# Kernel tuning notes

Hardware: AMD Instinct MI355X
Metric: run time of the kernel (lower is better)

The kernel has to match this reference:

```python
import jax, jax.numpy as jnp
import numpy as np

SCALE = 0.08838834764831845  # 1/sqrt(head_dim=128)


def setup_inputs() -> dict:
    key = jax.random.key(0)
    ks = jax.random.split(key, 5)
    B, H, D = 16, 8, 128          # batch (decode seqs), kv heads, head_dim
    BS, BPS = 16, 128             # block_size, blocks per sequence
    NBLK = B * BPS                # total cache blocks (2048)
    CTX = 2048                    # context length per sequence
    q = jax.random.normal(ks[0], (B, H, D), jnp.float32)
    k = jax.random.normal(ks[1], (B, H, D), jnp.float32)
    v = jax.random.normal(ks[2], (B, H, D), jnp.float32)
    k_cache = jax.random.normal(ks[3], (NBLK, BS, H, D), jnp.float32)
    v_cache = jax.random.normal(ks[4], (NBLK, BS, H, D), jnp.float32)
    # each sequence owns a distinct contiguous set of blocks
    block_tables = jnp.arange(B * BPS, dtype=jnp.int32).reshape(B, BPS)
    context_lens = jnp.full((B,), CTX, dtype=jnp.int32)
    # slot for the newest token (position CTX-1) of each sequence
    last = CTX - 1
    slot_mapping = block_tables[:, last // BS] * BS + (last % BS)
    return {"q": q, "k": k, "v": v, "k_cache": k_cache, "v_cache": v_cache,
            "slot_mapping": slot_mapping.astype(jnp.int32),
            "block_tables": block_tables, "context_lens": context_lens}


def reference(q, k, v, k_cache, v_cache, slot_mapping, block_tables, context_lens):
    # ---- store_kvcache: scatter new k/v tokens into paged caches ----
    nblk, bs, H, D = k_cache.shape
    k_cache = k_cache.reshape(nblk * bs, H, D).at[slot_mapping].set(k).reshape(nblk, bs, H, D)
    v_cache = v_cache.reshape(nblk * bs, H, D).at[slot_mapping].set(v).reshape(nblk, bs, H, D)

    # ---- _sdpa_decode: paged gather + masked attention (q_per_seq = 1) ----
    B, nb = block_tables.shape
    T = nb * bs                              # max tokens per sequence
    token_idx = jnp.arange(T, dtype=jnp.int32)
    block_idx = token_idx // bs
    token_off = token_idx % bs
    block_ids = block_tables[:, block_idx]   # [B, T]
    k_all = k_cache[block_ids, token_off]    # [B, T, H, D]
    v_all = v_cache[block_ids, token_off]    # [B, T, H, D]

    valid = token_idx[None, :] < context_lens[:, None]           # [B, T]
    q_pos = context_lens - 1                                     # q_per_seq == 1
    causal = token_idx[None, :] <= q_pos[:, None]                # [B, T]
    mask = valid & causal

    scores = jnp.einsum("bhd,bthd->bht", q, k_all) * SCALE       # [B, H, T]
    scores = jnp.where(mask[:, None, :], scores, -jnp.inf)
    p = jax.nn.softmax(scores, axis=-1)
    out = jnp.einsum("bht,bthd->bhd", p, v_all)                  # [B, H, D]
    return out
```

## Files before the change

kernel.cpp:

```cpp
#include <hip/hip_runtime.h>
#include <math.h>

#define B_ 16
#define H_ 8
#define D_ 128
#define BS_ 16
#define BPS_ 128
#define T_ (BPS_ * BS_)
#define ROW_ (H_ * D_)
#define SCALE_ 0.08838834764831845f

template<int NS>
__global__ __launch_bounds__(256) void attn_partial(
    const float* __restrict__ q,
    const float* __restrict__ knew,
    const float* __restrict__ vnew,
    const float* __restrict__ kc,
    const float* __restrict__ vc,
    const int* __restrict__ btab,
    const int* __restrict__ clen,
    float* __restrict__ ws_m,
    float* __restrict__ ws_l,
    float* __restrict__ ws_o)
{
    constexpr int CHUNK = T_ / NS;
    constexpr int TPW = CHUNK / 4;
    constexpr int NBLK_C = CHUNK / BS_;

    const int c = blockIdx.x;
    const int b = blockIdx.y;
    const int tid = threadIdx.x;
    const int wave = tid >> 6;
    const int lane = tid & 63;
    const int hl = lane & 31;
    const int half = lane >> 5;
    const int ctx = clen[b];
    const int cs = c * CHUNK;

    __shared__ int   s_bt[NBLK_C];
    __shared__ float s_p[H_][CHUNK];
    __shared__ float s_mx[H_], s_l[H_];
    __shared__ float s_o[4][H_][D_];

    if (tid < NBLK_C) s_bt[tid] = btab[b * BPS_ + c * NBLK_C + tid];

    float4 q4[4];
    #pragma unroll
    for (int j = 0; j < 4; ++j)
        q4[j] = *(const float4*)(q + (size_t)b * ROW_ + j * 256 + half * 128 + 4 * hl);
    __syncthreads();

    #pragma unroll 4
    for (int i = 0; i < TPW; i += 2) {
        float4 k4[8];
        #pragma unroll
        for (int u = 0; u < 2; ++u) {
            const int t = wave * TPW + i + u;
            const int tg = cs + t;
            const int blk = s_bt[t >> 4];
            const float* rb = (tg == ctx - 1)
                ? (knew + (size_t)b * ROW_)
                : (kc + ((size_t)blk * BS_ + (tg & 15)) * ROW_);
            #pragma unroll
            for (int j = 0; j < 4; ++j)
                k4[u * 4 + j] = *(const float4*)(rb + j * 256 + half * 128 + 4 * hl);
        }
        #pragma unroll
        for (int u = 0; u < 2; ++u) {
            const int t = wave * TPW + i + u;
            const int tg = cs + t;
            #pragma unroll
            for (int j = 0; j < 4; ++j) {
                const float4 kv = k4[u * 4 + j];
                float s = q4[j].x * kv.x + q4[j].y * kv.y + q4[j].z * kv.z + q4[j].w * kv.w;
                s += __shfl_xor(s, 16);
                s += __shfl_xor(s, 8);
                s += __shfl_xor(s, 4);
                s += __shfl_xor(s, 2);
                s += __shfl_xor(s, 1);
                if (hl == 0) s_p[2 * j + half][t] = (tg < ctx) ? s * SCALE_ : -INFINITY;
            }
        }
    }
    __syncthreads();

    {
        const int h = tid >> 5;
        float m = -INFINITY;
        for (int t = hl; t < CHUNK; t += 32) m = fmaxf(m, s_p[h][t]);
        m = fmaxf(m, __shfl_xor(m, 16));
        m = fmaxf(m, __shfl_xor(m, 8));
        m = fmaxf(m, __shfl_xor(m, 4));
        m = fmaxf(m, __shfl_xor(m, 2));
        m = fmaxf(m, __shfl_xor(m, 1));
        if (hl == 0) s_mx[h] = fmaxf(m, -1e30f);
    }
    __syncthreads();
    {
        const int h = tid >> 5;
        const float mx = s_mx[h];
        float l = 0.f;
        for (int t = hl; t < CHUNK; t += 32) {
            const float p = __expf(s_p[h][t] - mx);
            s_p[h][t] = p;
            l += p;
        }
        l += __shfl_xor(l, 16);
        l += __shfl_xor(l, 8);
        l += __shfl_xor(l, 4);
        l += __shfl_xor(l, 2);
        l += __shfl_xor(l, 1);
        if (hl == 0) s_l[h] = l;
    }
    __syncthreads();

    float4 acc[4];
    #pragma unroll
    for (int j = 0; j < 4; ++j) acc[j] = make_float4(0.f, 0.f, 0.f, 0.f);
    #pragma unroll 4
    for (int i = 0; i < TPW; i += 2) {
        float4 v4[8];
        #pragma unroll
        for (int u = 0; u < 2; ++u) {
            const int t = wave * TPW + i + u;
            const int tg = cs + t;
            const int blk = s_bt[t >> 4];
            const float* rb = (tg == ctx - 1)
                ? (vnew + (size_t)b * ROW_)
                : (vc + ((size_t)blk * BS_ + (tg & 15)) * ROW_);
            #pragma unroll
            for (int j = 0; j < 4; ++j)
                v4[u * 4 + j] = *(const float4*)(rb + j * 256 + half * 128 + 4 * hl);
        }
        #pragma unroll
        for (int u = 0; u < 2; ++u) {
            const int t = wave * TPW + i + u;
            #pragma unroll
            for (int j = 0; j < 4; ++j) {
                const float pw = s_p[2 * j + half][t];
                acc[j].x += pw * v4[u * 4 + j].x;
                acc[j].y += pw * v4[u * 4 + j].y;
                acc[j].z += pw * v4[u * 4 + j].z;
                acc[j].w += pw * v4[u * 4 + j].w;
            }
        }
    }
    #pragma unroll
    for (int j = 0; j < 4; ++j)
        *(float4*)&s_o[wave][2 * j + half][4 * hl] = acc[j];
    __syncthreads();

    for (int r = tid; r < H_ * D_; r += 256) {
        const int h = r >> 7, d = r & 127;
        const float oo = s_o[0][h][d] + s_o[1][h][d] + s_o[2][h][d] + s_o[3][h][d];
        ws_o[((size_t)(b * H_ + h) * NS + c) * D_ + d] = oo;
    }
    if (tid < H_) {
        ws_m[(b * H_ + tid) * NS + c] = s_mx[tid];
        ws_l[(b * H_ + tid) * NS + c] = s_l[tid];
    }
}

template<int NS>
__global__ __launch_bounds__(128) void attn_reduce(
    const float* __restrict__ ws_m,
    const float* __restrict__ ws_l,
    const float* __restrict__ ws_o,
    float* __restrict__ out)
{
    const int bh = blockIdx.x;
    const int tid = threadIdx.x;

    __shared__ float s_co[NS];
    __shared__ float s_lg;

    if (tid < 64) {
        float m = -INFINITY;
        for (int cc = tid; cc < NS; cc += 64) m = fmaxf(m, ws_m[bh * NS + cc]);
        m = fmaxf(m, __shfl_xor(m, 32));
        m = fmaxf(m, __shfl_xor(m, 16));
        m = fmaxf(m, __shfl_xor(m, 8));
        m = fmaxf(m, __shfl_xor(m, 4));
        m = fmaxf(m, __shfl_xor(m, 2));
        m = fmaxf(m, __shfl_xor(m, 1));
        float lw = 0.f;
        for (int cc = tid; cc < NS; cc += 64) {
            const float co = __expf(ws_m[bh * NS + cc] - m);
            s_co[cc] = co;
            lw += ws_l[bh * NS + cc] * co;
        }
        lw += __shfl_xor(lw, 32);
        lw += __shfl_xor(lw, 16);
        lw += __shfl_xor(lw, 8);
        lw += __shfl_xor(lw, 4);
        lw += __shfl_xor(lw, 2);
        lw += __shfl_xor(lw, 1);
        if (tid == 0) s_lg = lw;
    }
    __syncthreads();

    float acc = 0.f;
    #pragma unroll 8
    for (int cc = 0; cc < NS; ++cc)
        acc += s_co[cc] * ws_o[((size_t)bh * NS + cc) * D_ + tid];
    out[(size_t)bh * D_ + tid] = acc / s_lg;
}

template<int NS>
static void launch_all(const float* q, const float* knew, const float* vnew,
                       const float* kc, const float* vc,
                       const int* btab, const int* clen,
                       float* ws, float* out, hipStream_t stream)
{
    float* ws_m = ws;
    float* ws_l = ws + B_ * H_ * NS;
    float* ws_o = ws + 2 * B_ * H_ * NS;
    attn_partial<NS><<<dim3(NS, B_), 256, 0, stream>>>(q, knew, vnew, kc, vc,
                                                       btab, clen, ws_m, ws_l, ws_o);
    attn_reduce<NS><<<dim3(B_ * H_), 128, 0, stream>>>(ws_m, ws_l, ws_o, out);
}

extern "C" void kernel_launch(void* const* d_in, const int* in_sizes, int n_in,
                              void* d_out, int out_size, void* d_ws, size_t ws_size,
                              hipStream_t stream) {
    const float* q    = (const float*)d_in[0];
    const float* knew = (const float*)d_in[1];
    const float* vnew = (const float*)d_in[2];
    const float* kc   = (const float*)d_in[3];
    const float* vc   = (const float*)d_in[4];
    const int* btab = (const int*)d_in[6];
    const int* clen = (const int*)d_in[7];
    float* out = (float*)d_out;
    float* ws  = (float*)d_ws;

    const size_t need64 = (size_t)B_ * H_ * 64 * (2 + D_) * sizeof(float);
    const size_t need32 = (size_t)B_ * H_ * 32 * (2 + D_) * sizeof(float);
    if (ws_size >= need64)      launch_all<64>(q, knew, vnew, kc, vc, btab, clen, ws, out, stream);
    else if (ws_size >= need32) launch_all<32>(q, knew, vnew, kc, vc, btab, clen, ws, out, stream);
    else                        launch_all<16>(q, knew, vnew, kc, vc, btab, clen, ws, out, stream);
}
```

Measured before the change: 292.5 us.

## Fuse K and V passes into single-pass online softmax with software-pipelined loads

Replaces the three-phase partial kernel (score pass over K, softmax over shared scores, then a second pass over V) with a single loop that loads K and V per token together and keeps per-wave online-softmax state (running max, sum, rescaled accumulator). Loads are double-buffered so the next token's K/V fetch overlaps the current token's compute, and per-wave partials are merged in shared memory with rescale coefficients. This removes the intermediate score buffer, several block barriers and the serialization between the K and V streams. In exchange it adds two exponentials per head per token and holds more registers, with launch_bounds raised to 4 blocks per CU.

```diff
diff --git a/kernel.cpp b/kernel.cpp
--- a/kernel.cpp
+++ b/kernel.cpp
@@ -11,7 +11,7 @@
 #define SCALE_ 0.08838834764831845f
 
 template<int NS>
-__global__ __launch_bounds__(256) void attn_partial(
+__global__ __launch_bounds__(256, 4) void attn_partial(
     const float* __restrict__ q,
     const float* __restrict__ knew,
     const float* __restrict__ vnew,
@@ -27,7 +27,7 @@
     constexpr int TPW = CHUNK / 4;
     constexpr int NBLK_C = CHUNK / BS_;
 
-    const int c = blockIdx.x;
+    const int cix = blockIdx.x;
     const int b = blockIdx.y;
     const int tid = threadIdx.x;
     const int wave = tid >> 6;
@@ -35,14 +35,14 @@
     const int hl = lane & 31;
     const int half = lane >> 5;
     const int ctx = clen[b];
-    const int cs = c * CHUNK;
+    const int cs = cix * CHUNK;
+    const int t0 = wave * TPW;
 
     __shared__ int   s_bt[NBLK_C];
-    __shared__ float s_p[H_][CHUNK];
-    __shared__ float s_mx[H_], s_l[H_];
-    __shared__ float s_o[4][H_][D_];
-
-    if (tid < NBLK_C) s_bt[tid] = btab[b * BPS_ + c * NBLK_C + tid];
+    __shared__ float s_m[4][H_], s_l[4][H_], s_c[4][H_];
+    __shared__ float s_oacc[4][H_][D_];
+
+    if (tid < NBLK_C) s_bt[tid] = btab[b * BPS_ + cix * NBLK_C + tid];
 
     float4 q4[4];
     #pragma unroll
@@ -50,114 +50,99 @@
         q4[j] = *(const float4*)(q + (size_t)b * ROW_ + j * 256 + half * 128 + 4 * hl);
     __syncthreads();
 
-    #pragma unroll 4
-    for (int i = 0; i < TPW; i += 2) {
-        float4 k4[8];
-        #pragma unroll
-        for (int u = 0; u < 2; ++u) {
-            const int t = wave * TPW + i + u;
-            const int tg = cs + t;
-            const int blk = s_bt[t >> 4];
-            const float* rb = (tg == ctx - 1)
-                ? (knew + (size_t)b * ROW_)
-                : (kc + ((size_t)blk * BS_ + (tg & 15)) * ROW_);
-            #pragma unroll
-            for (int j = 0; j < 4; ++j)
-                k4[u * 4 + j] = *(const float4*)(rb + j * 256 + half * 128 + 4 * hl);
-        }
-        #pragma unroll
-        for (int u = 0; u < 2; ++u) {
-            const int t = wave * TPW + i + u;
-            const int tg = cs + t;
-            #pragma unroll
-            for (int j = 0; j < 4; ++j) {
-                const float4 kv = k4[u * 4 + j];
-                float s = q4[j].x * kv.x + q4[j].y * kv.y + q4[j].z * kv.z + q4[j].w * kv.w;
-                s += __shfl_xor(s, 16);
-                s += __shfl_xor(s, 8);
-                s += __shfl_xor(s, 4);
-                s += __shfl_xor(s, 2);
-                s += __shfl_xor(s, 1);
-                if (hl == 0) s_p[2 * j + half][t] = (tg < ctx) ? s * SCALE_ : -INFINITY;
-            }
-        }
-    }
-    __syncthreads();
-
-    {
-        const int h = tid >> 5;
-        float m = -INFINITY;
-        for (int t = hl; t < CHUNK; t += 32) m = fmaxf(m, s_p[h][t]);
-        m = fmaxf(m, __shfl_xor(m, 16));
-        m = fmaxf(m, __shfl_xor(m, 8));
-        m = fmaxf(m, __shfl_xor(m, 4));
-        m = fmaxf(m, __shfl_xor(m, 2));
-        m = fmaxf(m, __shfl_xor(m, 1));
-        if (hl == 0) s_mx[h] = fmaxf(m, -1e30f);
-    }
-    __syncthreads();
-    {
-        const int h = tid >> 5;
-        const float mx = s_mx[h];
-        float l = 0.f;
-        for (int t = hl; t < CHUNK; t += 32) {
-            const float p = __expf(s_p[h][t] - mx);
-            s_p[h][t] = p;
-            l += p;
-        }
-        l += __shfl_xor(l, 16);
-        l += __shfl_xor(l, 8);
-        l += __shfl_xor(l, 4);
-        l += __shfl_xor(l, 2);
-        l += __shfl_xor(l, 1);
-        if (hl == 0) s_l[h] = l;
-    }
-    __syncthreads();
-
+    float m[4], l[4];
     float4 acc[4];
     #pragma unroll
-    for (int j = 0; j < 4; ++j) acc[j] = make_float4(0.f, 0.f, 0.f, 0.f);
-    #pragma unroll 4
-    for (int i = 0; i < TPW; i += 2) {
-        float4 v4[8];
-        #pragma unroll
-        for (int u = 0; u < 2; ++u) {
-            const int t = wave * TPW + i + u;
-            const int tg = cs + t;
-            const int blk = s_bt[t >> 4];
-            const float* rb = (tg == ctx - 1)
-                ? (vnew + (size_t)b * ROW_)
-                : (vc + ((size_t)blk * BS_ + (tg & 15)) * ROW_);
-            #pragma unroll
-            for (int j = 0; j < 4; ++j)
-                v4[u * 4 + j] = *(const float4*)(rb + j * 256 + half * 128 + 4 * hl);
-        }
-        #pragma unroll
-        for (int u = 0; u < 2; ++u) {
-            const int t = wave * TPW + i + u;
-            #pragma unroll
-            for (int j = 0; j < 4; ++j) {
-                const float pw = s_p[2 * j + half][t];
-                acc[j].x += pw * v4[u * 4 + j].x;
-                acc[j].y += pw * v4[u * 4 + j].y;
-                acc[j].z += pw * v4[u * 4 + j].z;
-                acc[j].w += pw * v4[u * 4 + j].w;
-            }
-        }
-    }
-    #pragma unroll
-    for (int j = 0; j < 4; ++j)
-        *(float4*)&s_o[wave][2 * j + half][4 * hl] = acc[j];
-    __syncthreads();
-
+    for (int j = 0; j < 4; ++j) {
+        m[j] = -1e30f;
+        l[j] = 0.f;
+        acc[j] = make_float4(0.f, 0.f, 0.f, 0.f);
+    }
+
+    auto load_tok = [&](int t, float4 (&kd)[4], float4 (&vd)[4]) {
+        const int tg = cs + t0 + t;
+        const int blk = s_bt[(t0 + t) >> 4];
+        const float* krb = (tg == ctx - 1)
+            ? (knew + (size_t)b * ROW_)
+            : (kc + ((size_t)blk * BS_ + (tg & 15)) * ROW_);
+        const float* vrb = (tg == ctx - 1)
+            ? (vnew + (size_t)b * ROW_)
+            : (vc + ((size_t)blk * BS_ + (tg & 15)) * ROW_);
+        #pragma unroll
+        for (int j = 0; j < 4; ++j) {
+            kd[j] = *(const float4*)(krb + j * 256 + half * 128 + 4 * hl);
+            vd[j] = *(const float4*)(vrb + j * 256 + half * 128 + 4 * hl);
+        }
+    };
+
+    auto compute = [&](int t, float4 (&kd)[4], float4 (&vd)[4]) {
+        const int tg = cs + t0 + t;
+        float s[4];
+        #pragma unroll
+        for (int j = 0; j < 4; ++j) {
+            float ss = q4[j].x * kd[j].x + q4[j].y * kd[j].y
+                     + q4[j].z * kd[j].z + q4[j].w * kd[j].w;
+            ss += __shfl_xor(ss, 16);
+            ss += __shfl_xor(ss, 8);
+            ss += __shfl_xor(ss, 4);
+            ss += __shfl_xor(ss, 2);
+            ss += __shfl_xor(ss, 1);
+            s[j] = (tg < ctx) ? ss * SCALE_ : -INFINITY;
+        }
+        #pragma unroll
+        for (int j = 0; j < 4; ++j) {
+            const float mn = fmaxf(m[j], s[j]);
+            const float al = __expf(m[j] - mn);
+            const float p  = __expf(s[j] - mn);
+            m[j] = mn;
+            l[j] = l[j] * al + p;
+            acc[j].x = acc[j].x * al + p * vd[j].x;
+            acc[j].y = acc[j].y * al + p * vd[j].y;
+            acc[j].z = acc[j].z * al + p * vd[j].z;
+            acc[j].w = acc[j].w * al + p * vd[j].w;
+        }
+    };
+
+    float4 kA[4], vA[4], kB[4], vB[4];
+    load_tok(0, kA, vA);
+    #pragma unroll
+    for (int tt = 0; tt < TPW / 2; ++tt) {
+        load_tok(2 * tt + 1, kB, vB);
+        compute(2 * tt, kA, vA);
+        if (2 * tt + 2 < TPW) load_tok(2 * tt + 2, kA, vA);
+        compute(2 * tt + 1, kB, vB);
+    }
+
+    #pragma unroll
+    for (int j = 0; j < 4; ++j) {
+        *(float4*)&s_oacc[wave][2 * j + half][4 * hl] = acc[j];
+        if (hl == 0) {
+            s_m[wave][2 * j + half] = m[j];
+            s_l[wave][2 * j + half] = l[j];
+        }
+    }
+    __syncthreads();
+
+    if (tid < H_) {
+        const int h = tid;
+        float M = fmaxf(fmaxf(s_m[0][h], s_m[1][h]), fmaxf(s_m[2][h], s_m[3][h]));
+        float L = 0.f;
+        #pragma unroll
+        for (int w = 0; w < 4; ++w) {
+            const float cf = __expf(s_m[w][h] - M);
+            s_c[w][h] = cf;
+            L += s_l[w][h] * cf;
+        }
+        const int idx = (b * H_ + h) * NS + cix;
+        ws_m[idx] = M;
+        ws_l[idx] = L;
+    }
+    __syncthreads();
     for (int r = tid; r < H_ * D_; r += 256) {
         const int h = r >> 7, d = r & 127;
-        const float oo = s_o[0][h][d] + s_o[1][h][d] + s_o[2][h][d] + s_o[3][h][d];
-        ws_o[((size_t)(b * H_ + h) * NS + c) * D_ + d] = oo;
-    }
-    if (tid < H_) {
-        ws_m[(b * H_ + tid) * NS + c] = s_mx[tid];
-        ws_l[(b * H_ + tid) * NS + c] = s_l[tid];
+        const float oo = s_oacc[0][h][d] * s_c[0][h] + s_oacc[1][h][d] * s_c[1][h]
+                       + s_oacc[2][h][d] * s_c[2][h] + s_oacc[3][h][d] * s_c[3][h];
+        ws_o[((size_t)(b * H_ + h) * NS + cix) * D_ + d] = oo;
     }
 }
 
```

New measurement: 315.2 us. 1.08x slower.
